# Optimization experiments

Measured on AMD Instinct MI355X. Metric: run time of the kernel, lower is better.

Reference implementation:

```python
import jax, jax.numpy as jnp
import numpy as np

EMBED_DIM = 768
NUM_HEADS = 12
HEAD_DIM = EMBED_DIM // NUM_HEADS


def setup_inputs() -> dict:
    key = jax.random.key(0)
    ks = jax.random.split(key, 12)
    B, T, D, Hp, Wp = 4, 32, EMBED_DIM, 16, 16
    h = jax.random.normal(ks[0], (B, T, D, Hp, Wp), dtype=jnp.float32)
    u_enc = jax.random.uniform(ks[1], (B, T, D, Hp, Wp), dtype=jnp.float32)
    lam = jax.random.uniform(ks[2], (B, T, 1, Hp, Wp), dtype=jnp.float32)
    s = 1.0 / np.sqrt(D)
    Wq = jax.random.normal(ks[3], (D, D), dtype=jnp.float32) * s
    bq = jnp.zeros((D,), dtype=jnp.float32)
    Wk = jax.random.normal(ks[4], (D, D), dtype=jnp.float32) * s
    bk = jnp.zeros((D,), dtype=jnp.float32)
    Wv = jax.random.normal(ks[5], (D, D), dtype=jnp.float32) * s
    bv = jnp.zeros((D,), dtype=jnp.float32)
    Wo = jax.random.normal(ks[6], (D, D), dtype=jnp.float32) * s
    bo = jnp.zeros((D,), dtype=jnp.float32)
    return {"h": h, "u_enc": u_enc, "lam": lam,
            "Wq": Wq, "bq": bq, "Wk": Wk, "bk": bk,
            "Wv": Wv, "bv": bv, "Wo": Wo, "bo": bo}


def reference(h, u_enc, lam, Wq, bq, Wk, bk, Wv, bv, Wo, bo):
    B, T, D, Hp, Wp = h.shape
    S = Hp * Wp
    NH, HD = NUM_HEADS, HEAD_DIM
    # (B,T,D,Hp,Wp) -> (B*S, T, D)
    h_seq = jnp.transpose(h, (0, 3, 4, 1, 2)).reshape(B * S, T, D)
    u_seq = jnp.transpose(u_enc, (0, 3, 4, 1, 2)).reshape(B * S, T, D)
    lam_seq = jnp.transpose(lam, (0, 3, 4, 1, 2)).reshape(B * S, T)
    # projections (nn.Linear: x @ W.T + b)
    Q = (h_seq @ Wq.T + bq).reshape(B * S, T, NH, HD).transpose(0, 2, 1, 3)
    K = (h_seq @ Wk.T + bk).reshape(B * S, T, NH, HD).transpose(0, 2, 1, 3)
    V = (h_seq @ Wv.T + bv).reshape(B * S, T, NH, HD).transpose(0, 2, 1, 3)
    scores = jnp.einsum('bhqd,bhkd->bhqk', Q, K) / jnp.sqrt(jnp.float32(HD))
    # key-dependent uncertainty penalty: lam_j * mean_d(u_j)
    u_pen = lam_seq * u_seq.mean(axis=-1)  # (B*S, T)
    scores = scores - u_pen[:, None, None, :]
    attn = jax.nn.softmax(scores, axis=-1)  # dropout: eval mode (identity)
    out = jnp.einsum('bhqk,bhkd->bhqd', attn, V)
    out = out.transpose(0, 2, 1, 3).reshape(B * S, T, D)
    out = out @ Wo.T + bo
    return jnp.transpose(out.reshape(B, Hp, Wp, T, D), (0, 3, 4, 1, 2))
```

## Files before the change

### kernel.cpp

```cpp
#include <hip/hip_runtime.h>

typedef float   f32x4 __attribute__((ext_vector_type(4)));
typedef _Float16 f16x8 __attribute__((ext_vector_type(8)));

#define DEV static __device__ __forceinline__

#define BB 4
#define TT 32
#define DD 768
#define SS 256
#define NH 12
#define HD 64
#define NSLAB (BB*TT)
#define NSEQ  (BB*SS)
#define MTOK  (NSEQ*TT)
#define NQKV  (3*DD)

DEV void async_copy16(const _Float16* g, _Float16* l) {
  __builtin_amdgcn_global_load_lds(
      (const __attribute__((address_space(1))) unsigned int*)g,
      (__attribute__((address_space(3))) unsigned int*)l,
      16, 0, 0);
}

DEV int swz_chunk(int r, int kc) {
  return r * 4 + (kc ^ (r & 3) ^ ((r >> 2) & 3));
}

__global__ __launch_bounds__(256) void k_transpose_h(const float* __restrict__ h,
                                                     _Float16* __restrict__ A) {
  __shared__ _Float16 Tl[256 * 65];
  const int slab = blockIdx.x;
  const int d0   = blockIdx.y * 64;
  const int t    = threadIdx.x;
  const float4* hv = (const float4*)(h + (slab * DD + d0) * SS);
  #pragma unroll
  for (int i = 0; i < 16; ++i) {
    int dd = i * 4 + (t >> 6);
    int s4 = (t & 63) * 4;
    float4 v = hv[dd * 64 + (t & 63)];
    Tl[(s4 + 0) * 65 + dd] = (_Float16)v.x;
    Tl[(s4 + 1) * 65 + dd] = (_Float16)v.y;
    Tl[(s4 + 2) * 65 + dd] = (_Float16)v.z;
    Tl[(s4 + 3) * 65 + dd] = (_Float16)v.w;
  }
  __syncthreads();
  #pragma unroll
  for (int p = 0; p < 8; ++p) {
    int s  = p * 32 + (t >> 3);
    int dd = (t & 7) * 8;
    f16x8 val;
    #pragma unroll
    for (int j = 0; j < 8; ++j) val[j] = Tl[s * 65 + dd + j];
    *(f16x8*)(A + (slab * SS + s) * DD + d0 + dd) = val;
  }
}

__global__ __launch_bounds__(256) void k_convert_w(const float* __restrict__ Wq,
                                                   const float* __restrict__ Wk,
                                                   const float* __restrict__ Wv,
                                                   const float* __restrict__ Wo,
                                                   _Float16* __restrict__ WQKV,
                                                   _Float16* __restrict__ WoH) {
  int idx = blockIdx.x * 256 + threadIdx.x;
  int row = idx / 96;
  int c8  = (idx % 96) * 8;
  const float* src; _Float16* dst;
  if (row < 768)       { src = Wq + row * 768;          dst = WQKV + row * 768; }
  else if (row < 1536) { src = Wk + (row - 768) * 768;  dst = WQKV + row * 768; }
  else if (row < 2304) { src = Wv + (row - 1536) * 768; dst = WQKV + row * 768; }
  else                 { src = Wo + (row - 2304) * 768; dst = WoH  + (row - 2304) * 768; }
  float4 v0 = *(const float4*)(src + c8);
  float4 v1 = *(const float4*)(src + c8 + 4);
  f16x8 o;
  o[0]=(_Float16)v0.x; o[1]=(_Float16)v0.y; o[2]=(_Float16)v0.z; o[3]=(_Float16)v0.w;
  o[4]=(_Float16)v1.x; o[5]=(_Float16)v1.y; o[6]=(_Float16)v1.z; o[7]=(_Float16)v1.w;
  *(f16x8*)(dst + c8) = o;
}

__global__ __launch_bounds__(256) void k_upen(const float* __restrict__ u,
                                              const float* __restrict__ lam,
                                              float* __restrict__ upen) {
  int slab = blockIdx.x >> 2;
  int q    = blockIdx.x & 3;
  int s    = threadIdx.x;
  const float* base = u + (slab * DD + q * 192) * SS + s;
  float sum = 0.f;
  for (int d = 0; d < 192; ++d) sum += base[d * SS];
  int b = slab >> 5, tt = slab & 31;
  float l = lam[slab * SS + s];
  atomicAdd(&upen[(b * SS + s) * TT + tt], sum * l * (1.0f / 768.0f));
}

__global__ __launch_bounds__(256) void k_gemm_qkv(const _Float16* __restrict__ A,
                                                  const _Float16* __restrict__ Bw,
                                                  const float* __restrict__ bq,
                                                  const float* __restrict__ bk,
                                                  const float* __restrict__ bv,
                                                  _Float16* __restrict__ QKV) {
  __shared__ _Float16 As[128 * 32];
  __shared__ _Float16 Bs[128 * 32];
  const int mt = blockIdx.x & 255, nt = blockIdx.x >> 8;
  const int m0 = mt * 128, n0 = nt * 128;
  const int tid = threadIdx.x, w = tid >> 6, lane = tid & 63;
  const int wr = (w >> 1) * 64, wc = (w & 1) * 64;
  f32x4 acc[4][4] = {};
  for (int it = 0; it < 24; ++it) {
    const int k0 = it * 32;
    __syncthreads();
    #pragma unroll
    for (int i = 0; i < 2; ++i) {
      int c = tid + 256 * i;
      int row = c >> 2;
      int coff = ((c & 3) ^ (row & 3) ^ ((row >> 2) & 3)) * 8;
      _Float16* ldsA = (_Float16*)((char*)As + w * 1024 + i * 4096 + lane * 16);
      _Float16* ldsB = (_Float16*)((char*)Bs + w * 1024 + i * 4096 + lane * 16);
      async_copy16(A  + (m0 + row) * DD + k0 + coff, ldsA);
      async_copy16(Bw + (n0 + row) * DD + k0 + coff, ldsB);
    }
    __syncthreads();
    f16x8 af[4], bf[4];
    #pragma unroll
    for (int mi = 0; mi < 4; ++mi)
      af[mi] = *(const f16x8*)&As[swz_chunk(wr + mi * 16 + (lane & 15), lane >> 4) * 8];
    #pragma unroll
    for (int ni = 0; ni < 4; ++ni)
      bf[ni] = *(const f16x8*)&Bs[swz_chunk(wc + ni * 16 + (lane & 15), lane >> 4) * 8];
    #pragma unroll
    for (int mi = 0; mi < 4; ++mi)
      #pragma unroll
      for (int ni = 0; ni < 4; ++ni)
        acc[mi][ni] = __builtin_amdgcn_mfma_f32_16x16x32_f16(af[mi], bf[ni], acc[mi][ni], 0, 0, 0);
  }
  #pragma unroll
  for (int ni = 0; ni < 4; ++ni) {
    int n = n0 + wc + ni * 16 + (lane & 15);
    float bias, scale = 1.0f;
    if (n < 768)       { bias = bq[n];        scale = 0.125f; }
    else if (n < 1536) { bias = bk[n - 768]; }
    else               { bias = bv[n - 1536]; }
    #pragma unroll
    for (int mi = 0; mi < 4; ++mi) {
      int mbase = m0 + wr + mi * 16 + (lane >> 4) * 4;
      f32x4 v = acc[mi][ni];
      #pragma unroll
      for (int r = 0; r < 4; ++r)
        QKV[(mbase + r) * NQKV + n] = (_Float16)((v[r] + bias) * scale);
    }
  }
}

__global__ __launch_bounds__(256) void k_attn(const _Float16* __restrict__ QKV,
                                              const float* __restrict__ upen,
                                              _Float16* __restrict__ O) {
  __shared__ _Float16 lds[4][32 * 64 + 32 * 40];
  const int w = threadIdx.x >> 6, lane = threadIdx.x & 63;
  const int seq = blockIdx.x / 3, hg = blockIdx.x % 3;
  const int head = hg * 4 + w;
  const int b = seq >> 8, s = seq & 255;
  _Float16* Vs = &lds[w][0];
  _Float16* Ps = &lds[w][32 * 64];
  const _Float16* qptr = QKV + head * HD;
  const _Float16* kptr = QKV + DD + head * HD;
  const _Float16* vptr = QKV + 2 * DD + head * HD;
  #define MROW(t_) ((((b << 5) + (t_)) * SS + s) * NQKV)

  #pragma unroll
  for (int p = 0; p < 4; ++p) {
    int t  = p * 8 + (lane >> 3);
    int cc = (lane & 7) * 8;
    *(f16x8*)(Vs + t * 64 + cc) = *(const f16x8*)(vptr + MROW(t) + cc);
  }
  f16x8 qf[2][2], kf[2][2];
  #pragma unroll
  for (int i = 0; i < 2; ++i)
    #pragma unroll
    for (int ks = 0; ks < 2; ++ks) {
      int t  = i * 16 + (lane & 15);
      int kk = ks * 32 + (lane >> 4) * 8;
      qf[i][ks] = *(const f16x8*)(qptr + MROW(t) + kk);
      kf[i][ks] = *(const f16x8*)(kptr + MROW(t) + kk);
    }
  f32x4 sc[2][2] = {};
  #pragma unroll
  for (int mq = 0; mq < 2; ++mq)
    #pragma unroll
    for (int nk = 0; nk < 2; ++nk)
      #pragma unroll
      for (int ks = 0; ks < 2; ++ks)
        sc[mq][nk] = __builtin_amdgcn_mfma_f32_16x16x32_f16(qf[mq][ks], kf[nk][ks], sc[mq][nk], 0, 0, 0);

  const float up0 = upen[seq * TT + (lane & 15)];
  const float up1 = upen[seq * TT + 16 + (lane & 15)];

  #pragma unroll
  for (int mq = 0; mq < 2; ++mq) {
    #pragma unroll
    for (int r = 0; r < 4; ++r) {
      float s0 = sc[mq][0][r] - up0;
      float s1 = sc[mq][1][r] - up1;
      float mx = fmaxf(s0, s1);
      #pragma unroll
      for (int off = 1; off < 16; off <<= 1) mx = fmaxf(mx, __shfl_xor(mx, off, 64));
      float e0 = __expf(s0 - mx), e1 = __expf(s1 - mx);
      float sum = e0 + e1;
      #pragma unroll
      for (int off = 1; off < 16; off <<= 1) sum += __shfl_xor(sum, off, 64);
      float inv = 1.0f / sum;
      int row = mq * 16 + (lane >> 4) * 4 + r;
      Ps[row * 40 + (lane & 15)]      = (_Float16)(e0 * inv);
      Ps[row * 40 + 16 + (lane & 15)] = (_Float16)(e1 * inv);
    }
  }
  f16x8 pf[2];
  #pragma unroll
  for (int mq = 0; mq < 2; ++mq)
    pf[mq] = *(const f16x8*)(Ps + (mq * 16 + (lane & 15)) * 40 + (lane >> 4) * 8);
  f32x4 oacc[2][4] = {};
  #pragma unroll
  for (int nh = 0; nh < 4; ++nh) {
    int hd = nh * 16 + (lane & 15);
    f16x8 vf;
    #pragma unroll
    for (int j = 0; j < 8; ++j) vf[j] = Vs[((lane >> 4) * 8 + j) * 64 + hd];
    #pragma unroll
    for (int mq = 0; mq < 2; ++mq)
      oacc[mq][nh] = __builtin_amdgcn_mfma_f32_16x16x32_f16(pf[mq], vf, oacc[mq][nh], 0, 0, 0);
  }
  #pragma unroll
  for (int mq = 0; mq < 2; ++mq)
    #pragma unroll
    for (int nh = 0; nh < 4; ++nh) {
      int hd = nh * 16 + (lane & 15);
      #pragma unroll
      for (int r = 0; r < 4; ++r) {
        int t = mq * 16 + (lane >> 4) * 4 + r;
        O[(((b << 5) + t) * SS + s) * DD + head * HD + hd] = (_Float16)oacc[mq][nh][r];
      }
    }
  #undef MROW
}

__global__ __launch_bounds__(256) void k_gemm_out(const _Float16* __restrict__ Wn,
                                                  const _Float16* __restrict__ O,
                                                  const float* __restrict__ bo,
                                                  float* __restrict__ out) {
  __shared__ _Float16 As[128 * 32];
  __shared__ _Float16 Bs[128 * 32];
  const int ct = blockIdx.x & 255, rt = blockIdx.x >> 8;
  const int R0 = rt * 128, C0 = ct * 128;
  const int tid = threadIdx.x, w = tid >> 6, lane = tid & 63;
  const int wr = (w >> 1) * 64, wc = (w & 1) * 64;
  f32x4 acc[4][4] = {};
  for (int it = 0; it < 24; ++it) {
    const int k0 = it * 32;
    __syncthreads();
    #pragma unroll
    for (int i = 0; i < 2; ++i) {
      int c = tid + 256 * i;
      int row = c >> 2;
      int coff = ((c & 3) ^ (row & 3) ^ ((row >> 2) & 3)) * 8;
      _Float16* ldsA = (_Float16*)((char*)As + w * 1024 + i * 4096 + lane * 16);
      _Float16* ldsB = (_Float16*)((char*)Bs + w * 1024 + i * 4096 + lane * 16);
      async_copy16(Wn + (R0 + row) * DD + k0 + coff, ldsA);
      async_copy16(O  + (C0 + row) * DD + k0 + coff, ldsB);
    }
    __syncthreads();
    f16x8 af[4], bf[4];
    #pragma unroll
    for (int ri = 0; ri < 4; ++ri)
      af[ri] = *(const f16x8*)&As[swz_chunk(wr + ri * 16 + (lane & 15), lane >> 4) * 8];
    #pragma unroll
    for (int ci = 0; ci < 4; ++ci)
      bf[ci] = *(const f16x8*)&Bs[swz_chunk(wc + ci * 16 + (lane & 15), lane >> 4) * 8];
    #pragma unroll
    for (int ri = 0; ri < 4; ++ri)
      #pragma unroll
      for (int ci = 0; ci < 4; ++ci)
        acc[ri][ci] = __builtin_amdgcn_mfma_f32_16x16x32_f16(af[ri], bf[ci], acc[ri][ci], 0, 0, 0);
  }
  const int slab  = C0 >> 8;
  const int sbase = C0 & 255;
  #pragma unroll
  for (int ri = 0; ri < 4; ++ri) {
    #pragma unroll
    for (int ci = 0; ci < 4; ++ci) {
      int s = sbase + wc + ci * 16 + (lane & 15);
      f32x4 v = acc[ri][ci];
      #pragma unroll
      for (int r = 0; r < 4; ++r) {
        int R = R0 + wr + ri * 16 + (lane >> 4) * 4 + r;
        out[(slab * DD + R) * SS + s] = v[r] + bo[R];
      }
    }
  }
}

extern "C" void kernel_launch(void* const* d_in, const int* in_sizes, int n_in,
                              void* d_out, int out_size, void* d_ws, size_t ws_size,
                              hipStream_t stream) {
  const float* h   = (const float*)d_in[0];
  const float* u   = (const float*)d_in[1];
  const float* lam = (const float*)d_in[2];
  const float* Wq  = (const float*)d_in[3];
  const float* bq  = (const float*)d_in[4];
  const float* Wk  = (const float*)d_in[5];
  const float* bk  = (const float*)d_in[6];
  const float* Wv  = (const float*)d_in[7];
  const float* bv  = (const float*)d_in[8];
  const float* Wo  = (const float*)d_in[9];
  const float* bo  = (const float*)d_in[10];
  float* out = (float*)d_out;

  char* ws = (char*)d_ws;
  _Float16* Abuf = (_Float16*)(ws);
  _Float16* WQKV = (_Float16*)(ws + 50331648);
  _Float16* WoH  = (_Float16*)(ws + 53870592);
  float*    upen = (float*)   (ws + 55050240);
  _Float16* QKV  = (_Float16*)(ws + 55181312);

  hipMemsetAsync(upen, 0, 32768 * sizeof(float), stream);
  k_transpose_h<<<dim3(128, 12), 256, 0, stream>>>(h, Abuf);
  k_convert_w<<<1152, 256, 0, stream>>>(Wq, Wk, Wv, Wo, WQKV, WoH);
  k_upen<<<512, 256, 0, stream>>>(u, lam, upen);
  k_gemm_qkv<<<256 * 18, 256, 0, stream>>>(Abuf, WQKV, bq, bk, bv, QKV);
  k_attn<<<1024 * 3, 256, 0, stream>>>(QKV, upen, Abuf);
  k_gemm_out<<<256 * 6, 256, 0, stream>>>(WoH, Abuf, bo, out);
}
```

Before: 533.9 us.

## Widen GEMM tiles to 128x256 and write Q/K/V in per-head contiguous layout

Both GEMMs now use 128x256 block tiles with 4x8 MFMA accumulators per wave, and launch_bounds(256,2), so each loaded tile feeds more MFMAs. The QKV GEMM epilogue scatters into separate Q, K and V buffers laid out per (sequence, head) as contiguous 32x64 blocks. This lets the attention kernel read Q, K and V with contiguous loads. V is staged in LDS with a padded stride of 66 to reduce bank conflicts on the column reads. The costs are higher register pressure, a scattered epilogue write pattern in the QKV GEMM, and fewer blocks in the grid.

```diff
diff --git a/kernel.cpp b/kernel.cpp
--- a/kernel.cpp
+++ b/kernel.cpp
@@ -9,12 +9,10 @@
 #define TT 32
 #define DD 768
 #define SS 256
-#define NH 12
+#define NHD 12
 #define HD 64
-#define NSLAB (BB*TT)
 #define NSEQ  (BB*SS)
 #define MTOK  (NSEQ*TT)
-#define NQKV  (3*DD)
 
 DEV void async_copy16(const _Float16* g, _Float16* l) {
   __builtin_amdgcn_global_load_lds(
@@ -92,19 +90,21 @@
   atomicAdd(&upen[(b * SS + s) * TT + tt], sum * l * (1.0f / 768.0f));
 }
 
-__global__ __launch_bounds__(256) void k_gemm_qkv(const _Float16* __restrict__ A,
-                                                  const _Float16* __restrict__ Bw,
-                                                  const float* __restrict__ bq,
-                                                  const float* __restrict__ bk,
-                                                  const float* __restrict__ bv,
-                                                  _Float16* __restrict__ QKV) {
+__global__ __launch_bounds__(256, 2) void k_gemm_qkv(const _Float16* __restrict__ A,
+                                                     const _Float16* __restrict__ Bw,
+                                                     const float* __restrict__ bq,
+                                                     const float* __restrict__ bk,
+                                                     const float* __restrict__ bv,
+                                                     _Float16* __restrict__ Qp,
+                                                     _Float16* __restrict__ Kp,
+                                                     _Float16* __restrict__ Vp) {
   __shared__ _Float16 As[128 * 32];
-  __shared__ _Float16 Bs[128 * 32];
+  __shared__ _Float16 Bs[256 * 32];
   const int mt = blockIdx.x & 255, nt = blockIdx.x >> 8;
-  const int m0 = mt * 128, n0 = nt * 128;
+  const int m0 = mt * 128, n0 = nt * 256;
   const int tid = threadIdx.x, w = tid >> 6, lane = tid & 63;
-  const int wr = (w >> 1) * 64, wc = (w & 1) * 64;
-  f32x4 acc[4][4] = {};
+  const int wr = (w >> 1) * 64, wcc = (w & 1) * 128;
+  f32x4 acc[4][8] = {};
   for (int it = 0; it < 24; ++it) {
     const int k0 = it * 32;
     __syncthreads();
@@ -113,73 +113,95 @@
       int c = tid + 256 * i;
       int row = c >> 2;
       int coff = ((c & 3) ^ (row & 3) ^ ((row >> 2) & 3)) * 8;
-      _Float16* ldsA = (_Float16*)((char*)As + w * 1024 + i * 4096 + lane * 16);
-      _Float16* ldsB = (_Float16*)((char*)Bs + w * 1024 + i * 4096 + lane * 16);
-      async_copy16(A  + (m0 + row) * DD + k0 + coff, ldsA);
+      _Float16* ldsA = (_Float16*)((char*)As + (w * 1024 + i * 4096 + lane * 16));
+      async_copy16(A + (m0 + row) * DD + k0 + coff, ldsA);
+    }
+    #pragma unroll
+    for (int i = 0; i < 4; ++i) {
+      int c = tid + 256 * i;
+      int row = c >> 2;
+      int coff = ((c & 3) ^ (row & 3) ^ ((row >> 2) & 3)) * 8;
+      _Float16* ldsB = (_Float16*)((char*)Bs + (w * 1024 + i * 4096 + lane * 16));
       async_copy16(Bw + (n0 + row) * DD + k0 + coff, ldsB);
     }
     __syncthreads();
-    f16x8 af[4], bf[4];
+    f16x8 af[4], bf[8];
     #pragma unroll
     for (int mi = 0; mi < 4; ++mi)
       af[mi] = *(const f16x8*)&As[swz_chunk(wr + mi * 16 + (lane & 15), lane >> 4) * 8];
     #pragma unroll
-    for (int ni = 0; ni < 4; ++ni)
-      bf[ni] = *(const f16x8*)&Bs[swz_chunk(wc + ni * 16 + (lane & 15), lane >> 4) * 8];
+    for (int ni = 0; ni < 8; ++ni)
+      bf[ni] = *(const f16x8*)&Bs[swz_chunk(wcc + ni * 16 + (lane & 15), lane >> 4) * 8];
     #pragma unroll
     for (int mi = 0; mi < 4; ++mi)
       #pragma unroll
-      for (int ni = 0; ni < 4; ++ni)
+      for (int ni = 0; ni < 8; ++ni)
         acc[mi][ni] = __builtin_amdgcn_mfma_f32_16x16x32_f16(af[mi], bf[ni], acc[mi][ni], 0, 0, 0);
   }
-  #pragma unroll
-  for (int ni = 0; ni < 4; ++ni) {
-    int n = n0 + wc + ni * 16 + (lane & 15);
-    float bias, scale = 1.0f;
-    if (n < 768)       { bias = bq[n];        scale = 0.125f; }
-    else if (n < 1536) { bias = bk[n - 768]; }
-    else               { bias = bv[n - 1536]; }
+  const int sel = nt / 3;
+  const float scale = (sel == 0) ? 0.125f : 1.0f;
+  const float* bias = (sel == 0) ? bq : ((sel == 1) ? bk : bv);
+  _Float16* dst = (sel == 0) ? Qp : ((sel == 1) ? Kp : Vp);
+  const int slab = mt >> 1, s0 = (mt & 1) * 128;
+  const int b = slab >> 5, t = slab & 31;
+  #pragma unroll
+  for (int ni = 0; ni < 8; ++ni) {
+    int n768 = nt * 256 - sel * 768 + wcc + ni * 16 + (lane & 15);
+    int head = n768 >> 6, hd = n768 & 63;
+    float bs = bias[n768];
+    long hb = (long)head * 2048 + t * 64 + hd;
     #pragma unroll
     for (int mi = 0; mi < 4; ++mi) {
-      int mbase = m0 + wr + mi * 16 + (lane >> 4) * 4;
       f32x4 v = acc[mi][ni];
       #pragma unroll
-      for (int r = 0; r < 4; ++r)
-        QKV[(mbase + r) * NQKV + n] = (_Float16)((v[r] + bias) * scale);
-    }
-  }
-}
-
-__global__ __launch_bounds__(256) void k_attn(const _Float16* __restrict__ QKV,
+      for (int r = 0; r < 4; ++r) {
+        int s = s0 + wr + mi * 16 + (lane >> 4) * 4 + r;
+        long seq = b * 256 + s;
+        dst[seq * 24576 + hb] = (_Float16)((v[r] + bs) * scale);
+      }
+    }
+  }
+}
+
+__global__ __launch_bounds__(256) void k_attn(const _Float16* __restrict__ Qp,
+                                              const _Float16* __restrict__ Kp,
+                                              const _Float16* __restrict__ Vp,
                                               const float* __restrict__ upen,
                                               _Float16* __restrict__ O) {
-  __shared__ _Float16 lds[4][32 * 64 + 32 * 40];
+  __shared__ _Float16 lds[4][32 * 66 + 32 * 40];
   const int w = threadIdx.x >> 6, lane = threadIdx.x & 63;
   const int seq = blockIdx.x / 3, hg = blockIdx.x % 3;
   const int head = hg * 4 + w;
   const int b = seq >> 8, s = seq & 255;
   _Float16* Vs = &lds[w][0];
-  _Float16* Ps = &lds[w][32 * 64];
-  const _Float16* qptr = QKV + head * HD;
-  const _Float16* kptr = QKV + DD + head * HD;
-  const _Float16* vptr = QKV + 2 * DD + head * HD;
-  #define MROW(t_) ((((b << 5) + (t_)) * SS + s) * NQKV)
-
-  #pragma unroll
-  for (int p = 0; p < 4; ++p) {
-    int t  = p * 8 + (lane >> 3);
-    int cc = (lane & 7) * 8;
-    *(f16x8*)(Vs + t * 64 + cc) = *(const f16x8*)(vptr + MROW(t) + cc);
+  _Float16* Ps = &lds[w][32 * 66];
+  const long base = (long)(seq * NHD + head) * 2048;
+  const _Float16* Qb = Qp + base;
+  const _Float16* Kb = Kp + base;
+  const _Float16* Vb = Vp + base;
+
+  {
+    int t = lane & 31, hh = (lane >> 5) * 32;
+    f16x8 vc[4];
+    #pragma unroll
+    for (int c = 0; c < 4; ++c) vc[c] = *(const f16x8*)(Vb + t * 64 + hh + c * 8);
+    #pragma unroll
+    for (int c = 0; c < 4; ++c)
+      #pragma unroll
+      for (int p = 0; p < 4; ++p) {
+        union { _Float16 h[2]; unsigned u; } pk;
+        pk.h[0] = vc[c][2 * p]; pk.h[1] = vc[c][2 * p + 1];
+        *(unsigned*)&Vs[t * 66 + hh + c * 8 + 2 * p] = pk.u;
+      }
   }
   f16x8 qf[2][2], kf[2][2];
   #pragma unroll
   for (int i = 0; i < 2; ++i)
     #pragma unroll
     for (int ks = 0; ks < 2; ++ks) {
-      int t  = i * 16 + (lane & 15);
-      int kk = ks * 32 + (lane >> 4) * 8;
-      qf[i][ks] = *(const f16x8*)(qptr + MROW(t) + kk);
-      kf[i][ks] = *(const f16x8*)(kptr + MROW(t) + kk);
+      int off = (i * 16 + (lane & 15)) * 64 + ks * 32 + (lane >> 4) * 8;
+      qf[i][ks] = *(const f16x8*)(Qb + off);
+      kf[i][ks] = *(const f16x8*)(Kb + off);
     }
   f32x4 sc[2][2] = {};
   #pragma unroll
@@ -222,7 +244,7 @@
     int hd = nh * 16 + (lane & 15);
     f16x8 vf;
     #pragma unroll
-    for (int j = 0; j < 8; ++j) vf[j] = Vs[((lane >> 4) * 8 + j) * 64 + hd];
+    for (int j = 0; j < 8; ++j) vf[j] = Vs[((lane >> 4) * 8 + j) * 66 + hd];
     #pragma unroll
     for (int mq = 0; mq < 2; ++mq)
       oacc[mq][nh] = __builtin_amdgcn_mfma_f32_16x16x32_f16(pf[mq], vf, oacc[mq][nh], 0, 0, 0);
@@ -235,23 +257,22 @@
       #pragma unroll
       for (int r = 0; r < 4; ++r) {
         int t = mq * 16 + (lane >> 4) * 4 + r;
-        O[(((b << 5) + t) * SS + s) * DD + head * HD + hd] = (_Float16)oacc[mq][nh][r];
+        O[((long)((b << 5) + t) * SS + s) * DD + head * HD + hd] = (_Float16)oacc[mq][nh][r];
       }
     }
-  #undef MROW
-}
-
-__global__ __launch_bounds__(256) void k_gemm_out(const _Float16* __restrict__ Wn,
-                                                  const _Float16* __restrict__ O,
-                                                  const float* __restrict__ bo,
-                                                  float* __restrict__ out) {
+}
+
+__global__ __launch_bounds__(256, 2) void k_gemm_out(const _Float16* __restrict__ Wn,
+                                                     const _Float16* __restrict__ O,
+                                                     const float* __restrict__ bo,
+                                                     float* __restrict__ out) {
   __shared__ _Float16 As[128 * 32];
-  __shared__ _Float16 Bs[128 * 32];
-  const int ct = blockIdx.x & 255, rt = blockIdx.x >> 8;
-  const int R0 = rt * 128, C0 = ct * 128;
+  __shared__ _Float16 Bs[256 * 32];
+  const int ct = blockIdx.x & 127, rt = blockIdx.x >> 7;
+  const int R0 = rt * 128, C0 = ct * 256;
   const int tid = threadIdx.x, w = tid >> 6, lane = tid & 63;
-  const int wr = (w >> 1) * 64, wc = (w & 1) * 64;
-  f32x4 acc[4][4] = {};
+  const int wr = (w >> 1) * 64, wcc = (w & 1) * 128;
+  f32x4 acc[4][8] = {};
   for (int it = 0; it < 24; ++it) {
     const int k0 = it * 32;
     __syncthreads();
@@ -260,37 +281,42 @@
       int c = tid + 256 * i;
       int row = c >> 2;
       int coff = ((c & 3) ^ (row & 3) ^ ((row >> 2) & 3)) * 8;
-      _Float16* ldsA = (_Float16*)((char*)As + w * 1024 + i * 4096 + lane * 16);
-      _Float16* ldsB = (_Float16*)((char*)Bs + w * 1024 + i * 4096 + lane * 16);
+      _Float16* ldsA = (_Float16*)((char*)As + (w * 1024 + i * 4096 + lane * 16));
       async_copy16(Wn + (R0 + row) * DD + k0 + coff, ldsA);
-      async_copy16(O  + (C0 + row) * DD + k0 + coff, ldsB);
+    }
+    #pragma unroll
+    for (int i = 0; i < 4; ++i) {
+      int c = tid + 256 * i;
+      int row = c >> 2;
+      int coff = ((c & 3) ^ (row & 3) ^ ((row >> 2) & 3)) * 8;
+      _Float16* ldsB = (_Float16*)((char*)Bs + (w * 1024 + i * 4096 + lane * 16));
+      async_copy16(O + (C0 + row) * DD + k0 + coff, ldsB);
     }
     __syncthreads();
-    f16x8 af[4], bf[4];
+    f16x8 af[4], bf[8];
     #pragma unroll
     for (int ri = 0; ri < 4; ++ri)
       af[ri] = *(const f16x8*)&As[swz_chunk(wr + ri * 16 + (lane & 15), lane >> 4) * 8];
     #pragma unroll
-    for (int ci = 0; ci < 4; ++ci)
-      bf[ci] = *(const f16x8*)&Bs[swz_chunk(wc + ci * 16 + (lane & 15), lane >> 4) * 8];
+    for (int ci = 0; ci < 8; ++ci)
+      bf[ci] = *(const f16x8*)&Bs[swz_chunk(wcc + ci * 16 + (lane & 15), lane >> 4) * 8];
     #pragma unroll
     for (int ri = 0; ri < 4; ++ri)
       #pragma unroll
-      for (int ci = 0; ci < 4; ++ci)
+      for (int ci = 0; ci < 8; ++ci)
         acc[ri][ci] = __builtin_amdgcn_mfma_f32_16x16x32_f16(af[ri], bf[ci], acc[ri][ci], 0, 0, 0);
   }
-  const int slab  = C0 >> 8;
-  const int sbase = C0 & 255;
+  const int slab = ct;
   #pragma unroll
   for (int ri = 0; ri < 4; ++ri) {
     #pragma unroll
-    for (int ci = 0; ci < 4; ++ci) {
-      int s = sbase + wc + ci * 16 + (lane & 15);
+    for (int ci = 0; ci < 8; ++ci) {
+      int s = wcc + ci * 16 + (lane & 15);
       f32x4 v = acc[ri][ci];
       #pragma unroll
       for (int r = 0; r < 4; ++r) {
         int R = R0 + wr + ri * 16 + (lane >> 4) * 4 + r;
-        out[(slab * DD + R) * SS + s] = v[r] + bo[R];
+        out[((long)slab * DD + R) * SS + s] = v[r] + bo[R];
       }
     }
   }
@@ -317,13 +343,15 @@
   _Float16* WQKV = (_Float16*)(ws + 50331648);
   _Float16* WoH  = (_Float16*)(ws + 53870592);
   float*    upen = (float*)   (ws + 55050240);
-  _Float16* QKV  = (_Float16*)(ws + 55181312);
+  _Float16* Qp   = (_Float16*)(ws + 55181312);
+  _Float16* Kp   = (_Float16*)(ws + 105512960);
+  _Float16* Vp   = (_Float16*)(ws + 155844608);
 
   hipMemsetAsync(upen, 0, 32768 * sizeof(float), stream);
   k_transpose_h<<<dim3(128, 12), 256, 0, stream>>>(h, Abuf);
   k_convert_w<<<1152, 256, 0, stream>>>(Wq, Wk, Wv, Wo, WQKV, WoH);
   k_upen<<<512, 256, 0, stream>>>(u, lam, upen);
-  k_gemm_qkv<<<256 * 18, 256, 0, stream>>>(Abuf, WQKV, bq, bk, bv, QKV);
-  k_attn<<<1024 * 3, 256, 0, stream>>>(QKV, upen, Abuf);
-  k_gemm_out<<<256 * 6, 256, 0, stream>>>(WoH, Abuf, bo, out);
-}
+  k_gemm_qkv<<<256 * 9, 256, 0, stream>>>(Abuf, WQKV, bq, bk, bv, Qp, Kp, Vp);
+  k_attn<<<1024 * 3, 256, 0, stream>>>(Qp, Kp, Vp, upen, Abuf);
+  k_gemm_out<<<128 * 6, 256, 0, stream>>>(WoH, Abuf, bo, out);
+}
```

Result: no change. 533.7 us (-0.0%).
